# Kernel tuning notes

Hardware: AMD Instinct MI355X
Metric: run time of the kernel (lower is better)

The kernel has to match this reference:

```python
import jax, jax.numpy as jnp
import numpy as np

SEQ_LEN = 2048
DIM = 1024
K = 24
N_FFT = 4096  # nearest power of two >= 2*seq_len - 1


def setup_inputs() -> dict:
    key = jax.random.key(0)
    k1, k2, k3, k4 = jax.random.split(key, 4)
    x = jax.random.normal(k1, (4, SEQ_LEN, DIM), dtype=jnp.float32)
    filters = jax.random.normal(k2, (SEQ_LEN, K), dtype=jnp.float32) * 0.1
    M_inputs = jax.random.normal(k3, (DIM, DIM), dtype=jnp.float32) * (DIM ** -0.5)
    M_filters = jax.random.normal(k4, (K, DIM), dtype=jnp.float32) * (K ** -0.5)
    input_pos = jnp.arange(SEQ_LEN, dtype=jnp.int32)
    return {"x": x, "filters": filters, "M_inputs": M_inputs,
            "M_filters": M_filters, "input_pos": input_pos}


def reference(x, filters, M_inputs, M_filters, input_pos):
    # STU forward, use_approx=True, use_hankel_L=False, no flash_fft, no cache.
    B, S, D = x.shape
    # alternating sign +1,-1,+1,... along sequence
    sgn = jnp.where(jnp.arange(S) % 2 == 0, 1.0, -1.0).astype(x.dtype)[None, :, None]
    x_proj = x @ M_inputs                      # (B, S, D)
    phi_proj = filters @ M_filters             # (S, D)
    # v: (1, S, D, 1) -> rfft over seq axis with length N_FFT
    V = jnp.fft.rfft(phi_proj[None, :, :, None], n=N_FFT, axis=1)
    # U: stack [u, u*sgn] on last axis -> (B, S, D, 2)
    U = jnp.fft.rfft(jnp.stack([x_proj, x_proj * sgn], axis=-1), n=N_FFT, axis=1)
    U_conv = jnp.fft.irfft(V * U, n=N_FFT, axis=1)[:, :S]   # (B, S, D, 2)
    spectral_plus = U_conv[..., 0]
    spectral_minus = U_conv[..., 1] * sgn
    return spectral_plus + spectral_minus
```

## Files before the change

kernel.cpp:

```cpp
#include <hip/hip_runtime.h>
#include <hip/hip_bf16.h>
#include <stdint.h>
#include <stddef.h>

#define DIM 1024
#define SEQ 2048
#define KF 24

using f32x4    = __attribute__((ext_vector_type(4))) float;
using bf16x8   = __attribute__((ext_vector_type(8))) short;
using uint32x4 = __attribute__((ext_vector_type(4))) unsigned int;

__device__ __forceinline__ unsigned short f2bf(float f){
  union { float f; unsigned int i; } v; v.f = f;
  unsigned int r = v.i + 0x7FFFu + ((v.i >> 16) & 1u);
  return (unsigned short)(r >> 16);
}
__device__ __forceinline__ float dot2bf(unsigned int a, unsigned int b, float c){
  float d;
  asm("v_dot2_f32_bf16 %0, %1, %2, %3" : "=v"(d) : "v"(a), "v"(b), "v"(c));
  return d;
}
__device__ __forceinline__ unsigned vext(const uint32x4 v, int i){
  return i == 0 ? v.x : i == 1 ? v.y : i == 2 ? v.z : v.w;
}
__device__ __forceinline__ void gload_lds16(const void* g, void* l){
  __builtin_amdgcn_global_load_lds(
      (const __attribute__((address_space(1))) unsigned int*)g,
      (__attribute__((address_space(3))) unsigned int*)l, 16, 0, 0);
}
__device__ __forceinline__ uint32x4 make_srsrc(const void* base, unsigned bytes){
  uint32x4 r;
  r.x = (unsigned)(uintptr_t)base;
  r.y = (unsigned)((uintptr_t)base >> 32);
  r.z = bytes;
  r.w = 0x00020000u;
  return r;
}

__global__ void k_cvt_x(const float* __restrict__ x, unsigned short* __restrict__ xb){
  int i = blockIdx.x * 256 + threadIdx.x;
  const float4* x4 = (const float4*)x;
  float4 v = x4[i];
  ushort4 o;
  o.x = f2bf(v.x); o.y = f2bf(v.y); o.z = f2bf(v.z); o.w = f2bf(v.w);
  *(ushort4*)(xb + (size_t)i * 4) = o;
}

__global__ void k_tr_M(const float* __restrict__ Mi, unsigned short* __restrict__ MbT){
  __shared__ float tile[32][33];
  int e0 = blockIdx.y * 32, d0 = blockIdx.x * 32;
  int tx = threadIdx.x, ty = threadIdx.y;
  #pragma unroll
  for (int r = 0; r < 32; r += 8)
    tile[ty + r][tx] = Mi[(size_t)(e0 + ty + r) * DIM + d0 + tx];
  __syncthreads();
  #pragma unroll
  for (int r = 0; r < 32; r += 8)
    MbT[(size_t)(d0 + ty + r) * DIM + e0 + tx] = f2bf(tile[tx][ty + r]);
}

__global__ void k_pe(const float* __restrict__ filters, const float* __restrict__ Mf,
                     unsigned int* __restrict__ pepkT){
  int r2 = blockIdx.x * 256 + threadIdx.x;
  int d  = blockIdx.y;
  float a0 = 0.f, a1 = 0.f;
  #pragma unroll
  for (int k = 0; k < KF; ++k){
    float mf = Mf[(size_t)k * DIM + d];
    a0 += filters[(size_t)(4 * r2)     * KF + k] * mf;
    a1 += filters[(size_t)(4 * r2 + 2) * KF + k] * mf;
  }
  unsigned int lo = f2bf(2.f * a0), hi = f2bf(2.f * a1);
  pepkT[(size_t)d * 512 + r2] = lo | (hi << 16);
}

#define BM 128
#define BN 128
#define BKK 64
__global__ void k_gemm(const unsigned short* __restrict__ A,
                       const unsigned short* __restrict__ Bt,
                       unsigned int* __restrict__ Bg){
  __shared__ unsigned short As[BM * BKK];
  __shared__ unsigned short Bs[BN * BKK];
  int tid  = threadIdx.x;
  int lane = tid & 63, wave = tid >> 6;
  int wm = wave >> 1, wn = wave & 1;
  int trow0 = blockIdx.x * BM;
  int ncol0 = blockIdx.y * BN;

  f32x4 acc[4][4] = {};

  for (int kt = 0; kt < 1024 / BKK; ++kt){
    __syncthreads();
    #pragma unroll
    for (int g = 0; g < 4; ++g){
      int c  = wave * 4 + g;
      int mr = c * 8 + (lane >> 3);
      int u  = lane & 7;
      int su = u ^ (mr & 7);
      const unsigned short* srcA = A + (size_t)(trow0 + mr) * 1024 + kt * BKK + su * 8;
      gload_lds16(srcA, (char*)As + c * 1024);
      const unsigned short* srcB = Bt + (size_t)(ncol0 + mr) * 1024 + kt * BKK + su * 8;
      gload_lds16(srcB, (char*)Bs + c * 1024);
    }
    __syncthreads();

    bf16x8 af[4][2], bfr[4][2];
    #pragma unroll
    for (int mi = 0; mi < 4; ++mi){
      int row = wm * 64 + mi * 16 + (lane & 15);
      #pragma unroll
      for (int ks = 0; ks < 2; ++ks){
        int u = ((lane >> 4) + 4 * ks) ^ (row & 7);
        af[mi][ks] = *(const bf16x8*)((const char*)As + row * 128 + u * 16);
      }
    }
    #pragma unroll
    for (int ni = 0; ni < 4; ++ni){
      int row = wn * 64 + ni * 16 + (lane & 15);
      #pragma unroll
      for (int ks = 0; ks < 2; ++ks){
        int u = ((lane >> 4) + 4 * ks) ^ (row & 7);
        bfr[ni][ks] = *(const bf16x8*)((const char*)Bs + row * 128 + u * 16);
      }
    }
    #pragma unroll
    for (int mi = 0; mi < 4; ++mi)
      #pragma unroll
      for (int ni = 0; ni < 4; ++ni)
        #pragma unroll
        for (int ks = 0; ks < 2; ++ks)
          acc[mi][ni] = __builtin_amdgcn_mfma_f32_16x16x32_bf16(
              af[mi][ks], bfr[ni][ks], acc[mi][ni], 0, 0, 0);
  }

  unsigned short* Bh = (unsigned short*)Bg;
  #pragma unroll
  for (int mi = 0; mi < 4; ++mi)
    #pragma unroll
    for (int ni = 0; ni < 4; ++ni){
      int col = ncol0 + wn * 64 + ni * 16 + (lane & 15);
      #pragma unroll
      for (int reg = 0; reg < 4; ++reg){
        int row = trow0 + wm * 64 + mi * 16 + (lane >> 4) * 4 + reg;
        unsigned short y = f2bf(acc[mi][ni][reg]);
        int t = row & 2047, bq = row >> 11;
        int p = t & 1, j = t >> 1;
        size_t strm = ((size_t)bq * 2 + p) * 1048576;
        size_t e_lo = strm + (size_t)(j >> 2) * 4096 + (size_t)col * 4 + (j & 3);
        if (j == 0) Bg[e_lo] = (unsigned int)y;
        else        Bh[2 * e_lo] = y;
        if (j < 1023){
          int j1 = j + 1;
          size_t e_hi = strm + (size_t)(j1 >> 2) * 4096 + (size_t)col * 4 + (j1 & 3);
          Bh[2 * e_hi + 1] = y;
        }
      }
    }
}

#define BLX4(dst, so) \
  asm volatile("buffer_load_dwordx4 %0, %1, %2, %3 offen" \
               : "=v"(dst) : "v"(voff), "s"(xrsrc), "s"(so))
#define BLP4_0(dst, so) \
  asm volatile("buffer_load_dwordx4 %0, %1, %2, %3 offen" \
               : "=v"(dst) : "v"(pvoff), "s"(prsrc), "s"(so))
#define BLP4_16(dst, so) \
  asm volatile("buffer_load_dwordx4 %0, %1, %2, %3 offen offset:16" \
               : "=v"(dst) : "v"(pvoff), "s"(prsrc), "s"(so))

__device__ __forceinline__ void phase_old(const uint32x4* XBO, const uint32x4* pv,
                                          float* acc){
  #pragma unroll
  for (int q = 0; q < 8; ++q)
    #pragma unroll
    for (int m = 0; m < 32; ++m){
      int idx = m - 2 * q + 16;
      if (idx >= 2 && idx < 16)
        acc[m] = dot2bf(vext(pv[q >> 2], q & 3), vext(XBO[(idx >> 2) & 3], idx & 3),
                        acc[m]);
    }
}
__device__ __forceinline__ void phase_mid_new(const uint32x4* XBM, const uint32x4* XBN,
                                              const uint32x4* pv, float* acc){
  #pragma unroll
  for (int q = 0; q < 8; ++q)
    #pragma unroll
    for (int m = 0; m < 32; ++m){
      int idx = m - 2 * q + 16;
      if (idx >= 16){
        unsigned w = (idx < 32) ? vext(XBM[(idx >> 2) & 3], idx & 3)
                                : vext(XBN[(idx >> 2) & 3], idx & 3);
        acc[m] = dot2bf(vext(pv[q >> 2], q & 3), w, acc[m]);
      }
    }
}

#define BODY(XBO_, XBM_, XBN_, C) do{                                            \
  phase_old(XBO_, pv, acc);                                                      \
  __builtin_amdgcn_sched_barrier(0);                                             \
  { unsigned _xs = (unsigned)(4 * (C) + 4) * 16384u;                             \
    BLX4(XBO_[0], _xs);                                                          \
    BLX4(XBO_[1], _xs + 16384u);                                                 \
    BLX4(XBO_[2], _xs + 32768u);                                                 \
    BLX4(XBO_[3], _xs + 49152u);                                                 \
    unsigned _ps = pbase - 32u * (unsigned)((C) + 1);                            \
    BLP4_0(npv[0], _ps); BLP4_16(npv[1], _ps); }                                 \
  __builtin_amdgcn_sched_barrier(0);                                             \
  phase_mid_new(XBM_, XBN_, pv, acc);                                            \
  asm volatile("s_waitcnt vmcnt(0)" ::: "memory");                               \
  __builtin_amdgcn_sched_barrier(0);                                             \
  pv[0] = npv[0]; pv[1] = npv[1];                                                \
}while(0)

__global__ __launch_bounds__(256, 4)
void k_conv(const unsigned int* __restrict__ Bg,
            const unsigned int* __restrict__ pepkT,
            float* __restrict__ out){
  int tid  = threadIdx.x;
  int bid  = blockIdx.x;
  int bp   = bid & 7;
  int rest = bid >> 3;
  int dblk = rest & 3;
  int mt   = 31 - (rest >> 2);
  int b = bp >> 1, p = bp & 1;
  int d = dblk * 256 + tid;

  uint32x4 xrsrc = make_srsrc(Bg + (size_t)bp * 1048576, 4194304u);
  uint32x4 prsrc = make_srsrc(pepkT, 2097152u);

  unsigned voff  = (unsigned)(d * 16);
  unsigned pvoff = (unsigned)(d * 2048);

  uint32x4 B0[4], B1[4], B2[4], pv[2], npv[2];
  float acc[32];

  unsigned pbase = 64u * (unsigned)mt + 32u;
  int nch = 2 * mt + 2;

  #pragma unroll
  for (int m = 0; m < 32; ++m) acc[m] = 0.f;

  #pragma unroll
  for (int k = 0; k < 4; ++k) BLX4(B0[k], (unsigned)(k - 8) * 16384u);
  #pragma unroll
  for (int k = 0; k < 4; ++k) BLX4(B1[k], (unsigned)(k - 4) * 16384u);
  #pragma unroll
  for (int k = 0; k < 4; ++k) BLX4(B2[k], (unsigned)k * 16384u);
  BLP4_0(pv[0], pbase); BLP4_16(pv[1], pbase);
  asm volatile("s_waitcnt vmcnt(0)" ::: "memory");
  __builtin_amdgcn_sched_barrier(0);

  int c = 0;
  for (;;){
    BODY(B0, B1, B2, c); if (++c == nch) break;
    BODY(B1, B2, B0, c); if (++c == nch) break;
    BODY(B2, B0, B1, c); if (++c == nch) break;
  }

  float* oc = out + ((size_t)(b * SEQ + p) * 1024 + d) + (size_t)mt * 32 * 2048;
  #pragma unroll
  for (int m = 0; m < 32; ++m) oc[(size_t)m * 2048] = acc[m];
}

extern "C" void kernel_launch(void* const* d_in, const int* in_sizes, int n_in,
                              void* d_out, int out_size, void* d_ws, size_t ws_size,
                              hipStream_t stream){
  const float* x       = (const float*)d_in[0];
  const float* filters = (const float*)d_in[1];
  const float* Mi      = (const float*)d_in[2];
  const float* Mf      = (const float*)d_in[3];

  char* ws = (char*)d_ws;
  unsigned short* Xb    = (unsigned short*)(ws);
  unsigned int*   Bg    = (unsigned int*)  (ws + (size_t)16 * 1024 * 1024);
  unsigned short* MbT   = (unsigned short*)(ws + (size_t)48 * 1024 * 1024);
  unsigned int*   pepkT = (unsigned int*)  (ws + (size_t)50 * 1024 * 1024);
  float* out = (float*)d_out;

  hipLaunchKernelGGL(k_cvt_x, dim3(8192), dim3(256), 0, stream, x, Xb);
  hipLaunchKernelGGL(k_tr_M,  dim3(32, 32), dim3(32, 8), 0, stream, Mi, MbT);
  hipLaunchKernelGGL(k_pe,    dim3(2, 1024), dim3(256), 0, stream, filters, Mf, pepkT);
  hipLaunchKernelGGL(k_gemm,  dim3(64, 8), dim3(256), 0, stream, Xb, MbT, Bg);
  hipLaunchKernelGGL(k_conv,  dim3(1024), dim3(256), 65536, stream, Bg, pepkT, out);
}
```

Measured before the change: 134.6 us.

## Deepen conv register pipeline to prefetch two chunks ahead

```diff
diff --git a/kernel.cpp b/kernel.cpp
--- a/kernel.cpp
+++ b/kernel.cpp
@@ -197,24 +197,23 @@
     }
 }
 
-#define BODY(XBO_, XBM_, XBN_, C) do{                                            \
-  phase_old(XBO_, pv, acc);                                                      \
+#define BODY4(XBO_, XBM_, XBN_, PVU_, PVL_, C) do{                               \
+  phase_old(XBO_, PVU_, acc);                                                    \
   __builtin_amdgcn_sched_barrier(0);                                             \
-  { unsigned _xs = (unsigned)(4 * (C) + 4) * 16384u;                             \
+  { unsigned _xs = (unsigned)(4 * (C) + 8) * 16384u;              \
     BLX4(XBO_[0], _xs);                                                          \
     BLX4(XBO_[1], _xs + 16384u);                                                 \
     BLX4(XBO_[2], _xs + 32768u);                                                 \
     BLX4(XBO_[3], _xs + 49152u);                                                 \
-    unsigned _ps = pbase - 32u * (unsigned)((C) + 1);                            \
-    BLP4_0(npv[0], _ps); BLP4_16(npv[1], _ps); }                                 \
+    unsigned _ps = pbase - 32u * (unsigned)((C) + 2);          \
+    BLP4_0(PVL_[0], _ps); BLP4_16(PVL_[1], _ps); }                               \
   __builtin_amdgcn_sched_barrier(0);                                             \
-  phase_mid_new(XBM_, XBN_, pv, acc);                                            \
-  asm volatile("s_waitcnt vmcnt(0)" ::: "memory");                               \
+  phase_mid_new(XBM_, XBN_, PVU_, acc);                                          \
+  asm volatile("s_waitcnt vmcnt(6)" ::: "memory");                               \
   __builtin_amdgcn_sched_barrier(0);                                             \
-  pv[0] = npv[0]; pv[1] = npv[1];                                                \
 }while(0)
 
-__global__ __launch_bounds__(256, 4)
+__global__ __launch_bounds__(256, 3)
 void k_conv(const unsigned int* __restrict__ Bg,
             const unsigned int* __restrict__ pepkT,
             float* __restrict__ out){
@@ -233,7 +232,8 @@
   unsigned voff  = (unsigned)(d * 16);
   unsigned pvoff = (unsigned)(d * 2048);
 
-  uint32x4 B0[4], B1[4], B2[4], pv[2], npv[2];
+  uint32x4 B0[4], B1[4], B2[4], B3[4];
+  uint32x4 pv0[2], pv1[2], pv2[2], pv3[2];
   float acc[32];
 
   unsigned pbase = 64u * (unsigned)mt + 32u;
@@ -243,20 +243,24 @@
   for (int m = 0; m < 32; ++m) acc[m] = 0.f;
 
   #pragma unroll
-  for (int k = 0; k < 4; ++k) BLX4(B0[k], (unsigned)(k - 8) * 16384u);
-  #pragma unroll
-  for (int k = 0; k < 4; ++k) BLX4(B1[k], (unsigned)(k - 4) * 16384u);
-  #pragma unroll
-  for (int k = 0; k < 4; ++k) BLX4(B2[k], (unsigned)k * 16384u);
-  BLP4_0(pv[0], pbase); BLP4_16(pv[1], pbase);
+  for (int k = 0; k < 4; ++k) BLX4(B2[k], (unsigned)(k - 8) * 16384u);
+  #pragma unroll
+  for (int k = 0; k < 4; ++k) BLX4(B3[k], (unsigned)(k - 4) * 16384u);
+  #pragma unroll
+  for (int k = 0; k < 4; ++k) BLX4(B0[k], (unsigned)k * 16384u);
+  #pragma unroll
+  for (int k = 0; k < 4; ++k) BLX4(B1[k], (unsigned)(k + 4) * 16384u);
+  BLP4_0(pv0[0], pbase);        BLP4_16(pv0[1], pbase);
+  BLP4_0(pv1[0], pbase - 32u);  BLP4_16(pv1[1], pbase - 32u);
   asm volatile("s_waitcnt vmcnt(0)" ::: "memory");
   __builtin_amdgcn_sched_barrier(0);
 
   int c = 0;
   for (;;){
-    BODY(B0, B1, B2, c); if (++c == nch) break;
-    BODY(B1, B2, B0, c); if (++c == nch) break;
-    BODY(B2, B0, B1, c); if (++c == nch) break;
+    BODY4(B2, B3, B0, pv0, pv2, c); if (++c == nch) break;
+    BODY4(B3, B0, B1, pv1, pv3, c); if (++c == nch) break;
+    BODY4(B0, B1, B2, pv2, pv0, c); if (++c == nch) break;
+    BODY4(B1, B2, B3, pv3, pv1, c); if (++c == nch) break;
   }
 
   float* oc = out + ((size_t)(b * SEQ + p) * 1024 + d) + (size_t)mt * 32 * 2048;
@@ -283,5 +287,5 @@
   hipLaunchKernelGGL(k_tr_M,  dim3(32, 32), dim3(32, 8), 0, stream, Mi, MbT);
   hipLaunchKernelGGL(k_pe,    dim3(2, 1024), dim3(256), 0, stream, filters, Mf, pepkT);
   hipLaunchKernelGGL(k_gemm,  dim3(64, 8), dim3(256), 0, stream, Xb, MbT, Bg);
-  hipLaunchKernelGGL(k_conv,  dim3(1024), dim3(256), 65536, stream, Bg, pepkT, out);
-}
+  hipLaunchKernelGGL(k_conv,  dim3(1024), dim3(256), 0, stream, Bg, pepkT, out);
+}
```

Measured after the change: 139.0 us. 1.03x slower.
